# Kernel optimization log

Hardware: AMD Instinct MI355X
Metric: run time of the kernel (lower is better)

## Reference

```python
import jax, jax.numpy as jnp
import numpy as np

NUM_HEAD = 8
ATTN_DIM = 512
WINDOW_WIDTH = 31
HALF_WIN = WINDOW_WIDTH // 2  # symmetric band half-width
NEG_INF = -1e10


def setup_inputs() -> dict:
    key = jax.random.key(0)
    k0, k1, k2 = jax.random.split(key, 3)
    n, c, w = 4, 512, 2048
    out_dim = 512
    input_ = jax.random.normal(k0, (n, c, 1, w), dtype=jnp.float32)
    mask = jnp.ones((n, w), dtype=jnp.float32)  # 1 = valid key position
    # xavier-uniform-like init for the two linears, zero bias (as in the module)
    lim_in = np.sqrt(6.0 / (c + 3 * ATTN_DIM)).astype(np.float32)
    W_in = jax.random.uniform(k1, (3 * ATTN_DIM, c), jnp.float32, -lim_in, lim_in)
    b_in = jnp.zeros((3 * ATTN_DIM,), jnp.float32)
    lim_fc = np.sqrt(6.0 / (ATTN_DIM + out_dim)).astype(np.float32)
    W_fc = jax.random.uniform(k2, (out_dim, ATTN_DIM), jnp.float32, -lim_fc, lim_fc)
    b_fc = jnp.zeros((out_dim,), jnp.float32)
    return {"input_": input_, "mask": mask, "W_in": W_in, "b_in": b_in,
            "W_fc": W_fc, "b_fc": b_fc}


def reference(input_, mask, W_in, b_in, W_fc, b_fc):
    n, c, h, w = input_.shape  # h == 1
    d = ATTN_DIM // NUM_HEAD
    x = input_.reshape(n, c, w).transpose(0, 2, 1)          # [n, w, c]
    temp = x @ W_in.T + b_in                                # [n, w, 3A]
    temp = temp.transpose(0, 2, 1)                          # [n, 3A, w]
    # channel layout after chunk(num_head) then chunk(3): [h, {q,k,v}, d]
    qkv = temp.reshape(n, NUM_HEAD, 3, d, w)
    q, k, v = qkv[:, :, 0], qkv[:, :, 1], qkv[:, :, 2]      # each [n, H, d, w]
    scale = NUM_HEAD / ATTN_DIM                              # == 1/d_head
    attn = jnp.einsum('nhdi,nhdj->nhij', q, k) * scale       # [n, H, w, w]
    # windowed band mask combined with per-key padding mask (clip_mask/mha_mask)
    idx = jnp.arange(w)
    band = jnp.abs(idx[:, None] - idx[None, :]) <= HALF_WIN  # [w, w]
    valid = band[None, None, :, :] & (mask > 0.5)[:, None, None, :]
    attn = jnp.where(valid, attn, NEG_INF)                   # pre-softmax mask
    attn = jax.nn.softmax(attn, axis=-1)
    attn = jnp.where(valid, attn, 0.0)                       # post-softmax mask
    # dropout in eval mode (identity) for a deterministic reference
    out = jnp.einsum('nhdj,nhij->nhdi', v, attn)             # [n, H, d, w]
    out = out.reshape(n, ATTN_DIM, w).transpose(0, 2, 1)     # [n, w, A]
    out = out @ W_fc.T + b_fc                                # [n, w, out_dim]
    od = out.shape[-1]
    return out.transpose(0, 2, 1).reshape(n, od, 1, w)
```

## Files before the change

kernel.cpp:

```cpp
#include <hip/hip_runtime.h>
#include <hip/hip_bf16.h>
#include <math.h>

#define W_SEQ   2048
#define C_IN    512
#define N_BATCH 4
#define NHEAD   8
#define QKV_CH  1536
#define OUT_CH  512
#define ATTND   512

typedef __attribute__((ext_vector_type(8))) short bf16x8;
typedef __attribute__((ext_vector_type(8))) unsigned short u16x8;
typedef __attribute__((ext_vector_type(4))) float f32x4;

__device__ __forceinline__ void gld16(const void* g, void* l) {
    __builtin_amdgcn_global_load_lds((const __attribute__((address_space(1))) void*)g,
                                     (__attribute__((address_space(3))) void*)l, 16, 0, 0);
}
__device__ __forceinline__ unsigned short f2bf(float f) {
    unsigned u = __float_as_uint(f);
    return (unsigned short)((u + 0x7FFFu + ((u >> 16) & 1u)) >> 16);
}

__global__ __launch_bounds__(256) void prep_xw_k(const float* __restrict__ in,
                                                 unsigned short* __restrict__ xh,
                                                 const float* __restrict__ w1,
                                                 unsigned short* __restrict__ w1h, int n1_4,
                                                 const float* __restrict__ w2,
                                                 unsigned short* __restrict__ w2h, int n2_4)
{
    const int b = blockIdx.x;
    if (b < 1024) {
        __shared__ float ts[64][65];
        const int n  = b >> 8;
        const int rm = b & 255;
        const int i0 = (rm & 31) * 64;
        const int c0 = (rm >> 5) * 64;
        const int t  = threadIdx.x;
        const int tx = t & 63, ty = t >> 6;
        #pragma unroll
        for (int s = 0; s < 16; ++s) {
            const int c = s * 4 + ty;
            ts[c][tx] = in[((size_t)(n * C_IN + c0 + c)) * W_SEQ + i0 + tx];
        }
        __syncthreads();
        const int c8 = t & 7, il = t >> 3;
        #pragma unroll
        for (int s = 0; s < 2; ++s) {
            const int i = il + 32 * s;
            u16x8 hv;
            #pragma unroll
            for (int e = 0; e < 8; ++e) hv[e] = f2bf(ts[c8 * 8 + e][i]);
            *(u16x8*)(&xh[((size_t)(n * W_SEQ + i0 + i)) * C_IN + c0 + c8 * 8]) = hv;
        }
    } else {
        const int idx = (b - 1024) * 256 + threadIdx.x;
        if (idx < n1_4) {
            const float4 v = ((const float4*)w1)[idx];
            ushort4 h; h.x = f2bf(v.x); h.y = f2bf(v.y); h.z = f2bf(v.z); h.w = f2bf(v.w);
            ((ushort4*)w1h)[idx] = h;
        } else if (idx < n1_4 + n2_4) {
            const int j = idx - n1_4;
            const float4 v = ((const float4*)w2)[j];
            ushort4 h; h.x = f2bf(v.x); h.y = f2bf(v.y); h.z = f2bf(v.z); h.w = f2bf(v.w);
            ((ushort4*)w2h)[j] = h;
        }
    }
}

template<int EPI>
__global__ __launch_bounds__(256, 4) void gemm_bf16(
    const unsigned short* __restrict__ A, const unsigned short* __restrict__ B,
    const float* __restrict__ bias, void* __restrict__ Cv, const int ldc)
{
    __shared__ __align__(16) char sm[32768];
    const int t = threadIdx.x;
    const int l = t & 63, w = t >> 6;
    int bx, by;
    if (EPI == 0) {
        const int d = blockIdx.x;
        const int y8 = d & 7, r = d >> 3;
        bx = r % 12;
        by = (r / 12) * 8 + y8;
    } else {
        bx = blockIdx.x; by = blockIdx.y;
    }
    const int m0 = by * 128, n0 = bx * 128;
    const int wm = w >> 1, wn = w & 1;

    const int subrow = l >> 3;
    const int swz    = ((l & 7) ^ subrow) << 4;
    const char* pA = (const char*)A + (size_t)m0 * 1024 + swz;
    const char* pB = (const char*)B + (size_t)n0 * 1024 + swz;

    const int frow = l & 15;
    f32x4 acc[4][4] = {};

    for (int k0 = 0; k0 < 512; k0 += 64) {
        const int kb = k0 * 2;
        #pragma unroll
        for (int c = 0; c < 4; ++c) {
            const int q = 4 * w + c;
            const size_t roff = (size_t)(q * 8 + subrow) * 1024 + kb;
            gld16(pA + roff, sm +         q * 1024);
            gld16(pB + roff, sm + 16384 + q * 1024);
        }
        __syncthreads();
        #pragma unroll
        for (int kk = 0; kk < 2; ++kk) {
            const int cswz = (kk * 64 + ((l >> 4) << 4)) ^ ((l & 7) << 4);
            bf16x8 a[4], b[4];
            #pragma unroll
            for (int mi = 0; mi < 4; ++mi)
                a[mi] = *(const bf16x8*)(sm + (wm * 64 + mi * 16 + frow) * 128 + cswz);
            #pragma unroll
            for (int ni = 0; ni < 4; ++ni)
                b[ni] = *(const bf16x8*)(sm + 16384 + (wn * 64 + ni * 16 + frow) * 128 + cswz);
            #pragma unroll
            for (int mi = 0; mi < 4; ++mi)
                #pragma unroll
                for (int ni = 0; ni < 4; ++ni)
                    acc[mi][ni] = __builtin_amdgcn_mfma_f32_16x16x32_bf16(a[mi], b[ni], acc[mi][ni], 0, 0, 0);
        }
        __syncthreads();
    }

    const int g = l >> 4;
    #pragma unroll
    for (int mi = 0; mi < 4; ++mi) {
        #pragma unroll
        for (int ni = 0; ni < 4; ++ni) {
            const int colg = n0 + wn * 64 + ni * 16 + frow;
            #pragma unroll
            for (int r = 0; r < 4; ++r) {
                const int rowg = m0 + wm * 64 + mi * 16 + g * 4 + r;
                const float v = acc[mi][ni][r];
                if (EPI == 0) {
                    ((unsigned short*)Cv)[(size_t)rowg * ldc + colg] = f2bf(v + bias[colg]);
                } else {
                    const int nb = colg >> 11, ii = colg & (W_SEQ - 1);
                    ((float*)Cv)[((size_t)(nb * OUT_CH + rowg)) * W_SEQ + ii] = v + bias[rowg];
                }
            }
        }
    }
}

#define VT_OFF  13824
#define MSK_OFF 30208
#define SM_SZ   30592

__global__ __launch_bounds__(256, 4) void attn4_k(const unsigned short* __restrict__ qkv,
                                                  const float* __restrict__ mask,
                                                  unsigned short* __restrict__ aoh)
{
    __shared__ __align__(16) char sm[SM_SZ];
    const int t = threadIdx.x, l = t & 63, w = t >> 6;
    const int i0 = blockIdx.x * 64, h = blockIdx.y, n = blockIdx.z;
    const int lr = l & 15, lg = l >> 4;

    const char* tb = (const char*)qkv + ((size_t)n * W_SEQ * QKV_CH + h * 192) * 2;

    const int r8 = l >> 3, c8 = l & 7;
    #pragma unroll
    for (int it = 0; it < 3; ++it) {
        const int jl = w * 24 + it * 8 + r8;
        const int jg = i0 - 16 + jl;
        bf16x8 kv = {}, vv = {};
        if (jg >= 0 && jg < W_SEQ) {
            const char* rp = tb + (size_t)jg * 3072;
            kv = *(const bf16x8*)(rp + 128 + c8 * 16);
            vv = *(const bf16x8*)(rp + 256 + c8 * 16);
        }
        *(bf16x8*)(sm + jl * 144 + c8 * 16) = kv;
        const int J0 = jl >> 3;
        #pragma unroll
        for (int e = 0; e < 8; ++e) {
            const int d = c8 * 8 + e;
            const int fold = ((d >> 3) ^ d) & 7;
            *(unsigned short*)(sm + VT_OFF + d * 256 + (((J0 ^ fold) << 4) | ((jl & 7) * 2)))
                = (unsigned short)vv[e];
        }
    }
    bf16x8 qh[2];
    {
        const char* qrow = tb + (size_t)(i0 + w * 16 + lr) * 3072 + lg * 16;
        qh[0] = *(const bf16x8*)(qrow);
        qh[1] = *(const bf16x8*)(qrow + 64);
    }
    if (t < 96) {
        const int jg = i0 - 16 + t;
        *(float*)(sm + MSK_OFF + t * 4) = (jg >= 0 && jg < W_SEQ) ? mask[n * W_SEQ + jg] : 0.f;
    }
    __syncthreads();

    f32x4 sacc[6] = {};
    #pragma unroll
    for (int nf = 0; nf < 6; ++nf) {
        #pragma unroll
        for (int kk = 0; kk < 2; ++kk) {
            const bf16x8 kh = *(const bf16x8*)(sm + (nf * 16 + lr) * 144 + kk * 64 + lg * 16);
            sacc[nf] = __builtin_amdgcn_mfma_f32_16x16x32_bf16(qh[kk], kh, sacc[nf], 0, 0, 0);
        }
    }
    __syncthreads();

    float mv[6];
    #pragma unroll
    for (int nf = 0; nf < 6; ++nf)
        mv[nf] = *(const float*)(sm + MSK_OFF + (nf * 16 + lr) * 4);

    #pragma unroll
    for (int r = 0; r < 4; ++r) {
        const int ri = w * 16 + lg * 4 + r;
        float sv[6], mrow = -1.0e30f;
        #pragma unroll
        for (int nf = 0; nf < 6; ++nf) {
            const int jcol = nf * 16 + lr;
            const bool valid = (jcol > ri) && (jcol <= ri + 31) && (mv[nf] > 0.5f);
            const float s = valid ? sacc[nf][r] * 0.015625f : -1.0e30f;
            sv[nf] = s;
            mrow = fmaxf(mrow, s);
        }
        #pragma unroll
        for (int off = 1; off <= 8; off <<= 1) mrow = fmaxf(mrow, __shfl_xor(mrow, off));
        float ls = 0.f;
        #pragma unroll
        for (int nf = 0; nf < 6; ++nf) {
            float pp = __expf(sv[nf] - mrow);
            pp = (sv[nf] > -1.0e29f) ? pp : 0.f;
            sv[nf] = pp;
            ls += pp;
        }
        #pragma unroll
        for (int off = 1; off <= 8; off <<= 1) ls += __shfl_xor(ls, off);
        const float rinv = (ls > 0.f) ? 1.f / ls : 0.f;
        #pragma unroll
        for (int nf = 0; nf < 6; ++nf)
            *(unsigned short*)(sm + ri * 208 + (nf * 16 + lr) * 2) = f2bf(sv[nf] * rinv);
    }

    f32x4 oacc[4] = {};
    #pragma unroll
    for (int ks = 0; ks < 3; ++ks) {
        const bf16x8 pah = *(const bf16x8*)(sm + (w * 16 + lr) * 208 + ks * 64 + lg * 16);
        #pragma unroll
        for (int nf2 = 0; nf2 < 4; ++nf2) {
            const int dd = nf2 * 16 + lr;
            const int fold = ((dd >> 3) ^ dd) & 7;
            const bf16x8 vb = *(const bf16x8*)(sm + VT_OFF + dd * 256 + (((4 * ks + lg) ^ fold) << 4));
            oacc[nf2] = __builtin_amdgcn_mfma_f32_16x16x32_bf16(pah, vb, oacc[nf2], 0, 0, 0);
        }
    }

    #pragma unroll
    for (int nf2 = 0; nf2 < 4; ++nf2) {
        #pragma unroll
        for (int r = 0; r < 4; ++r) {
            const int ri = w * 16 + lg * 4 + r;
            aoh[((size_t)(n * W_SEQ + i0 + ri)) * ATTND + h * 64 + nf2 * 16 + lr] = f2bf(oacc[nf2][r]);
        }
    }
}

extern "C" void kernel_launch(void* const* d_in, const int* in_sizes, int n_in,
                              void* d_out, int out_size, void* d_ws, size_t ws_size,
                              hipStream_t stream)
{
    const float* input = (const float*)d_in[0];
    const float* mask  = (const float*)d_in[1];
    const float* W_in  = (const float*)d_in[2];
    const float* b_in  = (const float*)d_in[3];
    const float* W_fc  = (const float*)d_in[4];
    const float* b_fc  = (const float*)d_in[5];
    float* out = (float*)d_out;
    char* ws = (char*)d_ws;

    unsigned short* QKVh = (unsigned short*)ws;
    unsigned short* AOh  = (unsigned short*)(ws + 25165824);
    unsigned short* Winh = (unsigned short*)(ws + 33554432);
    unsigned short* Wfch = (unsigned short*)(ws + 35127296);
    unsigned short* Xh   = (unsigned short*)(ws + 35651584);

    prep_xw_k<<<dim3(2048), 256, 0, stream>>>(input, Xh,
                                              W_in, Winh, QKV_CH * C_IN / 4,
                                              W_fc, Wfch, OUT_CH * ATTND / 4);
    gemm_bf16<0><<<dim3(768), 256, 0, stream>>>(Xh, Winh, b_in, QKVh, QKV_CH);
    attn4_k<<<dim3(W_SEQ / 64, NHEAD, N_BATCH), 256, 0, stream>>>(QKVh, mask, AOh);
    gemm_bf16<1><<<dim3(8192 / 128, OUT_CH / 128), 256, 0, stream>>>(
        Wfch, AOh, b_fc, out, 0);
}
```

Measured before the change: 52.29 us.

## Fuse all stages into one persistent kernel with atomic grid barriers

Replaces the four separate launches (prep, QKV GEMM, windowed attention, output GEMM) with one persistent kernel of 1024 blocks that loops over work units and separates stages with atomic-counter grid barriers. It also folds the weight conversion into the input transpose blocks, so prep needs 1024 units instead of 2048. The aim is to remove launch gaps and inter-kernel drain between stages. The cost is a memset launch plus spin-wait barriers, and correctness relies on all 1024 blocks being co-resident (4 per CU on 256 CUs), which an occupancy query checks before falling back to separate kernels.

```diff
diff --git a/kernel.cpp b/kernel.cpp
--- a/kernel.cpp
+++ b/kernel.cpp
@@ -9,6 +9,8 @@
 #define QKV_CH  1536
 #define OUT_CH  512
 #define ATTND   512
+#define N1_4    (QKV_CH * C_IN / 4)
+#define N2_4    (OUT_CH * ATTND / 4)
 
 typedef __attribute__((ext_vector_type(8))) short bf16x8;
 typedef __attribute__((ext_vector_type(8))) unsigned short u16x8;
@@ -23,69 +25,63 @@
     return (unsigned short)((u + 0x7FFFu + ((u >> 16) & 1u)) >> 16);
 }
 
-__global__ __launch_bounds__(256) void prep_xw_k(const float* __restrict__ in,
-                                                 unsigned short* __restrict__ xh,
-                                                 const float* __restrict__ w1,
-                                                 unsigned short* __restrict__ w1h, int n1_4,
-                                                 const float* __restrict__ w2,
-                                                 unsigned short* __restrict__ w2h, int n2_4)
-{
-    const int b = blockIdx.x;
-    if (b < 1024) {
-        __shared__ float ts[64][65];
-        const int n  = b >> 8;
-        const int rm = b & 255;
-        const int i0 = (rm & 31) * 64;
-        const int c0 = (rm >> 5) * 64;
-        const int t  = threadIdx.x;
-        const int tx = t & 63, ty = t >> 6;
-        #pragma unroll
-        for (int s = 0; s < 16; ++s) {
-            const int c = s * 4 + ty;
-            ts[c][tx] = in[((size_t)(n * C_IN + c0 + c)) * W_SEQ + i0 + tx];
-        }
-        __syncthreads();
-        const int c8 = t & 7, il = t >> 3;
-        #pragma unroll
-        for (int s = 0; s < 2; ++s) {
-            const int i = il + 32 * s;
-            u16x8 hv;
-            #pragma unroll
-            for (int e = 0; e < 8; ++e) hv[e] = f2bf(ts[c8 * 8 + e][i]);
-            *(u16x8*)(&xh[((size_t)(n * W_SEQ + i0 + i)) * C_IN + c0 + c8 * 8]) = hv;
-        }
+__device__ __forceinline__ void grid_sync(unsigned* bar, unsigned target) {
+    __syncthreads();
+    if (threadIdx.x == 0) {
+        __threadfence();
+        atomicAdd(bar, 1u);
+        while (atomicAdd(bar, 0u) < target)
+            __builtin_amdgcn_s_sleep(8);
+        __threadfence();
+    }
+    __syncthreads();
+}
+
+__device__ __forceinline__ void prep_unit(char* sm, int b,
+    const float* __restrict__ input, unsigned short* __restrict__ Xh,
+    const float* __restrict__ W_in, unsigned short* __restrict__ Winh,
+    const float* __restrict__ W_fc, unsigned short* __restrict__ Wfch)
+{
+    const int t = threadIdx.x;
+    float (*ts)[65] = (float(*)[65])sm;
+    const int n  = b >> 8, rm = b & 255;
+    const int i0 = (rm & 31) * 64, c0 = (rm >> 5) * 64;
+    const int tx = t & 63, ty = t >> 6;
+    #pragma unroll
+    for (int s = 0; s < 16; ++s) {
+        const int c = s * 4 + ty;
+        ts[c][tx] = input[((size_t)(n * C_IN + c0 + c)) * W_SEQ + i0 + tx];
+    }
+    __syncthreads();
+    const int c8 = t & 7, il = t >> 3;
+    #pragma unroll
+    for (int s = 0; s < 2; ++s) {
+        const int i = il + 32 * s;
+        u16x8 hv;
+        #pragma unroll
+        for (int e = 0; e < 8; ++e) hv[e] = f2bf(ts[c8 * 8 + e][i]);
+        *(u16x8*)(&Xh[((size_t)(n * W_SEQ + i0 + i)) * C_IN + c0 + c8 * 8]) = hv;
+    }
+    const int idx = b * 256 + t;
+    if (idx < N1_4) {
+        const float4 v = ((const float4*)W_in)[idx];
+        ushort4 hh; hh.x = f2bf(v.x); hh.y = f2bf(v.y); hh.z = f2bf(v.z); hh.w = f2bf(v.w);
+        ((ushort4*)Winh)[idx] = hh;
     } else {
-        const int idx = (b - 1024) * 256 + threadIdx.x;
-        if (idx < n1_4) {
-            const float4 v = ((const float4*)w1)[idx];
-            ushort4 h; h.x = f2bf(v.x); h.y = f2bf(v.y); h.z = f2bf(v.z); h.w = f2bf(v.w);
-            ((ushort4*)w1h)[idx] = h;
-        } else if (idx < n1_4 + n2_4) {
-            const int j = idx - n1_4;
-            const float4 v = ((const float4*)w2)[j];
-            ushort4 h; h.x = f2bf(v.x); h.y = f2bf(v.y); h.z = f2bf(v.z); h.w = f2bf(v.w);
-            ((ushort4*)w2h)[j] = h;
-        }
+        const int j = idx - N1_4;
+        const float4 v = ((const float4*)W_fc)[j];
+        ushort4 hh; hh.x = f2bf(v.x); hh.y = f2bf(v.y); hh.z = f2bf(v.z); hh.w = f2bf(v.w);
+        ((ushort4*)Wfch)[j] = hh;
     }
 }
 
 template<int EPI>
-__global__ __launch_bounds__(256, 4) void gemm_bf16(
+__device__ __forceinline__ void gemm_body(char* sm, int bx, int by,
     const unsigned short* __restrict__ A, const unsigned short* __restrict__ B,
     const float* __restrict__ bias, void* __restrict__ Cv, const int ldc)
 {
-    __shared__ __align__(16) char sm[32768];
     const int t = threadIdx.x;
     const int l = t & 63, w = t >> 6;
-    int bx, by;
-    if (EPI == 0) {
-        const int d = blockIdx.x;
-        const int y8 = d & 7, r = d >> 3;
-        bx = r % 12;
-        by = (r / 12) * 8 + y8;
-    } else {
-        bx = blockIdx.x; by = blockIdx.y;
-    }
     const int m0 = by * 128, n0 = bx * 128;
     const int wm = w >> 1, wn = w & 1;
 
@@ -149,15 +145,13 @@
 
 #define VT_OFF  13824
 #define MSK_OFF 30208
-#define SM_SZ   30592
-
-__global__ __launch_bounds__(256, 4) void attn4_k(const unsigned short* __restrict__ qkv,
-                                                  const float* __restrict__ mask,
-                                                  unsigned short* __restrict__ aoh)
-{
-    __shared__ __align__(16) char sm[SM_SZ];
+
+__device__ __forceinline__ void attn_body(char* sm, int blk,
+    const unsigned short* __restrict__ qkv, const float* __restrict__ mask,
+    unsigned short* __restrict__ aoh)
+{
     const int t = threadIdx.x, l = t & 63, w = t >> 6;
-    const int i0 = blockIdx.x * 64, h = blockIdx.y, n = blockIdx.z;
+    const int i0 = (blk & 31) * 64, h = (blk >> 5) & 7, n = blk >> 8;
     const int lr = l & 15, lg = l >> 4;
 
     const char* tb = (const char*)qkv + ((size_t)n * W_SEQ * QKV_CH + h * 192) * 2;
@@ -264,6 +258,72 @@
     }
 }
 
+__global__ __launch_bounds__(256, 4) void fused_all_k(
+    const float* __restrict__ input, const float* __restrict__ mask,
+    const float* __restrict__ W_in,  const float* __restrict__ b_in,
+    const float* __restrict__ W_fc,  const float* __restrict__ b_fc,
+    float* __restrict__ out,
+    unsigned short* __restrict__ QKVh, unsigned short* __restrict__ AOh,
+    unsigned short* __restrict__ Winh, unsigned short* __restrict__ Wfch,
+    unsigned short* __restrict__ Xh, unsigned* __restrict__ bar)
+{
+    __shared__ __align__(16) char sm[32768];
+    const int G = gridDim.x;
+
+    for (int u = blockIdx.x; u < 1024; u += G) {
+        prep_unit(sm, u, input, Xh, W_in, Winh, W_fc, Wfch);
+        __syncthreads();
+    }
+    grid_sync(bar + 0, G);
+
+    for (int u = blockIdx.x; u < 768; u += G) {
+        const int y8 = u & 7, r = u >> 3;
+        gemm_body<0>(sm, r % 12, (r / 12) * 8 + y8, Xh, Winh, b_in, QKVh, QKV_CH);
+        __syncthreads();
+    }
+    grid_sync(bar + 16, G);
+
+    for (int u = blockIdx.x; u < 1024; u += G) {
+        attn_body(sm, u, QKVh, mask, AOh);
+        __syncthreads();
+    }
+    grid_sync(bar + 32, G);
+
+    for (int u = blockIdx.x; u < 256; u += G)
+        gemm_body<1>(sm, u >> 2, u & 3, Wfch, AOh, b_fc, out, 0);
+}
+
+__global__ __launch_bounds__(256, 4) void prep_sep_k(
+    const float* __restrict__ input, unsigned short* __restrict__ Xh,
+    const float* __restrict__ W_in, unsigned short* __restrict__ Winh,
+    const float* __restrict__ W_fc, unsigned short* __restrict__ Wfch)
+{
+    __shared__ __align__(16) char sm[32768];
+    prep_unit(sm, blockIdx.x, input, Xh, W_in, Winh, W_fc, Wfch);
+}
+__global__ __launch_bounds__(256, 4) void gemm1_sep_k(
+    const unsigned short* __restrict__ A, const unsigned short* __restrict__ B,
+    const float* __restrict__ bias, unsigned short* __restrict__ C)
+{
+    __shared__ __align__(16) char sm[32768];
+    const int d = blockIdx.x, y8 = d & 7, r = d >> 3;
+    gemm_body<0>(sm, r % 12, (r / 12) * 8 + y8, A, B, bias, C, QKV_CH);
+}
+__global__ __launch_bounds__(256, 4) void attn_sep_k(
+    const unsigned short* __restrict__ qkv, const float* __restrict__ mask,
+    unsigned short* __restrict__ aoh)
+{
+    __shared__ __align__(16) char sm[32768];
+    attn_body(sm, blockIdx.x, qkv, mask, aoh);
+}
+__global__ __launch_bounds__(256, 4) void gemm2_sep_k(
+    const unsigned short* __restrict__ A, const unsigned short* __restrict__ B,
+    const float* __restrict__ bias, float* __restrict__ out)
+{
+    __shared__ __align__(16) char sm[32768];
+    gemm_body<1>(sm, blockIdx.x >> 2, blockIdx.x & 3, A, B, bias, out, 0);
+}
+
 extern "C" void kernel_launch(void* const* d_in, const int* in_sizes, int n_in,
                               void* d_out, int out_size, void* d_ws, size_t ws_size,
                               hipStream_t stream)
@@ -282,12 +342,20 @@
     unsigned short* Winh = (unsigned short*)(ws + 33554432);
     unsigned short* Wfch = (unsigned short*)(ws + 35127296);
     unsigned short* Xh   = (unsigned short*)(ws + 35651584);
-
-    prep_xw_k<<<dim3(2048), 256, 0, stream>>>(input, Xh,
-                                              W_in, Winh, QKV_CH * C_IN / 4,
-                                              W_fc, Wfch, OUT_CH * ATTND / 4);
-    gemm_bf16<0><<<dim3(768), 256, 0, stream>>>(Xh, Winh, b_in, QKVh, QKV_CH);
-    attn4_k<<<dim3(W_SEQ / 64, NHEAD, N_BATCH), 256, 0, stream>>>(QKVh, mask, AOh);
-    gemm_bf16<1><<<dim3(8192 / 128, OUT_CH / 128), 256, 0, stream>>>(
-        Wfch, AOh, b_fc, out, 0);
-}
+    unsigned*       bar  = (unsigned*)(ws + 46137344);
+
+    int occ = 0;
+    hipOccupancyMaxActiveBlocksPerMultiprocessor(&occ, fused_all_k, 256, 0);
+
+    if (occ >= 4) {
+        hipMemsetAsync(bar, 0, 192, stream);
+        fused_all_k<<<dim3(1024), 256, 0, stream>>>(
+            input, mask, W_in, b_in, W_fc, b_fc, out,
+            QKVh, AOh, Winh, Wfch, Xh, bar);
+    } else {
+        prep_sep_k <<<dim3(1024), 256, 0, stream>>>(input, Xh, W_in, Winh, W_fc, Wfch);
+        gemm1_sep_k<<<dim3(768),  256, 0, stream>>>(Xh, Winh, b_in, QKVh);
+        attn_sep_k <<<dim3(1024), 256, 0, stream>>>(QKVh, mask, AOh);
+        gemm2_sep_k<<<dim3(256),  256, 0, stream>>>(Wfch, AOh, b_fc, out);
+    }
+}
```

New measurement: 50.44 us. -3.5%, faster.
